# Performance work log

Hardware: AMD Instinct MI355X
Metric: run time of the kernel (lower is better)

The kernel has to match this reference:

```python
import jax, jax.numpy as jnp
import numpy as np

B, T, D, H = 2, 2048, 1024, 16
HD = D // H  # head_dim = 64
ROPE_BASE = 10000.0


def _rope_cos_sin(seq_len, head_dim, dtype):
    # Llama-style RoPE tables: [T, head_dim] with freqs repeated over both halves
    inv_freq = 1.0 / (ROPE_BASE ** (jnp.arange(0, head_dim, 2, dtype=jnp.float32) / head_dim))
    t = jnp.arange(seq_len, dtype=jnp.float32)
    freqs = jnp.outer(t, inv_freq)            # [T, head_dim/2]
    emb = jnp.concatenate([freqs, freqs], -1)  # [T, head_dim]
    return jnp.cos(emb).astype(dtype), jnp.sin(emb).astype(dtype)


def _apply_rope(x, cos, sin):
    # x: [B, T, H, HD]; rotate-half convention
    d2 = x.shape[-1] // 2
    x1, x2 = x[..., :d2], x[..., d2:]
    rotated = jnp.concatenate([-x2, x1], axis=-1)
    c = cos[None, :, None, :]
    s = sin[None, :, None, :]
    return x * c + rotated * s


def setup_inputs() -> dict:
    key = jax.random.key(0)
    ks = jax.random.split(key, 5)
    scale = 0.02
    return {
        "x": jax.random.normal(ks[0], (B, T, D), dtype=jnp.float32),
        "w_q": jax.random.normal(ks[1], (D, D), dtype=jnp.float32) * scale,
        "w_k": jax.random.normal(ks[2], (D, D), dtype=jnp.float32) * scale,
        "w_v": jax.random.normal(ks[3], (D, D), dtype=jnp.float32) * scale,
        "w_o": jax.random.normal(ks[4], (D, D), dtype=jnp.float32) * scale,
    }


def reference(x, w_q, w_k, w_v, w_o):
    b, n, d_in = x.shape
    # QKV projections -> [b, n, H, HD]
    q = (x @ w_q).reshape(b, n, H, HD)
    k = (x @ w_k).reshape(b, n, H, HD)
    v = (x @ w_v).reshape(b, n, H, HD)
    cos, sin = _rope_cos_sin(n, HD, x.dtype)
    q = _apply_rope(q, cos, sin)
    k = _apply_rope(k, cos, sin)
    # causal attention, scores scaled by sqrt(head_dim)
    scores = jnp.einsum('bqhd,bkhd->bhqk', q, k) / jnp.sqrt(jnp.asarray(HD, x.dtype))
    causal = jnp.tril(jnp.ones((n, n), dtype=bool))
    scores = jnp.where(causal[None, None, :, :], scores, -jnp.inf)
    weights = jax.nn.softmax(scores, axis=-1)
    ctx = jnp.einsum('bhqk,bkhd->bqhd', weights, v).reshape(b, n, H * HD)
    return ctx @ w_o
```

## Files before the change

### kernel.cpp

```cpp
#include <hip/hip_runtime.h>
#include <hip/hip_bf16.h>
#include <cstdint>

using u16 = unsigned short;
typedef short bf16x8 __attribute__((ext_vector_type(8)));
typedef float f32x4 __attribute__((ext_vector_type(4)));
typedef float f32x16 __attribute__((ext_vector_type(16)));
typedef u16 u16x4 __attribute__((ext_vector_type(4)));
typedef u16 u16x8 __attribute__((ext_vector_type(8)));

__device__ __forceinline__ u16 f2bf(float f) {
  union { float f; uint32_t u; } v; v.f = f;
  uint32_t r = (v.u + 0x7fffu + ((v.u >> 16) & 1u)) >> 16;
  return (u16)r;
}

__device__ __forceinline__ float bf2f(u16 u) {
  union { uint32_t u; float f; } v; v.u = (uint32_t)u << 16; return v.f;
}

__device__ __forceinline__ void async16(const void* g, void* l) {
  __builtin_amdgcn_global_load_lds(
      (const __attribute__((address_space(1))) uint32_t*)g,
      (__attribute__((address_space(3))) uint32_t*)l, 16, 0, 0);
}

__device__ __forceinline__ uint32_t cvtpk(float a, float b) {
  uint32_t r;
  asm("v_cvt_pk_bf16_f32 %0, %1, %2" : "=v"(r) : "v"(a), "v"(b));
  return r;
}

__device__ __forceinline__ void plswap(uint32_t& a, uint32_t& b) {
  asm volatile("v_permlane32_swap_b32 %0, %1" : "+v"(a), "+v"(b));
}

__global__ __launch_bounds__(256) void prep_kernel(
    const float* __restrict__ x, const float* __restrict__ wq, const float* __restrict__ wk,
    const float* __restrict__ wv, const float* __restrict__ wo,
    u16* __restrict__ xb, u16* __restrict__ Wqt, u16* __restrict__ Wkt,
    u16* __restrict__ Wvt, u16* __restrict__ Wot) {
  __shared__ float tile[64][65];
  const int tid = threadIdx.x;
  const int bid = blockIdx.x;
  if (bid < 4096) {
    int i = (bid * 256 + tid) * 4;
    float4 v = *(const float4*)(x + i);
    u16x4 o;
    o[0] = f2bf(v.x); o[1] = f2bf(v.y); o[2] = f2bf(v.z); o[3] = f2bf(v.w);
    *(u16x4*)(xb + i) = o;
    return;
  }
  const int id = bid - 4096;
  const int wsel = id >> 8, sub = id & 255;
  const float* W = (wsel == 0) ? wq : (wsel == 1) ? wk : (wsel == 2) ? wv : wo;
  u16* Wt = (wsel == 0) ? Wqt : (wsel == 1) ? Wkt : (wsel == 2) ? Wvt : Wot;
  const int k0 = (sub & 15) * 64, n0 = (sub >> 4) * 64;
#pragma unroll
  for (int i = 0; i < 4; ++i) {
    int c = i * 256 + tid;
    int r = c >> 4, c4 = c & 15;
    float4 v = *(const float4*)(W + (size_t)(k0 + r) * 1024 + n0 + c4 * 4);
    tile[r][c4 * 4 + 0] = v.x; tile[r][c4 * 4 + 1] = v.y;
    tile[r][c4 * 4 + 2] = v.z; tile[r][c4 * 4 + 3] = v.w;
  }
  __syncthreads();
#pragma unroll
  for (int i = 0; i < 2; ++i) {
    int c = i * 256 + tid;
    int n = c >> 3, kc = c & 7;
    u16x8 o;
#pragma unroll
    for (int j = 0; j < 8; ++j) o[j] = f2bf(tile[kc * 8 + j][n]);
    *(u16x8*)(Wt + (size_t)(n0 + n) * 1024 + k0 + kc * 8) = o;
  }
}

__device__ __forceinline__ void stage_ab(const u16* A, const u16* Bt, int m0, int n0, int kt,
                                         u16* As, u16* Bs, int w, int lane) {
#pragma unroll
  for (int c = 0; c < 2; ++c) {
    int chunk = w * 128 + c * 64 + lane;
    int row = chunk >> 2, cc = chunk & 3;
    int koff = kt * 32 + ((cc ^ (row & 3)) << 3);
    const u16* ga = A + (size_t)(m0 + row) * 1024 + koff;
    async16(ga, As + (size_t)(w * 128 + c * 64) * 8);
    const u16* gb = Bt + (size_t)(n0 + row) * 1024 + koff;
    async16(gb, Bs + (size_t)(w * 128 + c * 64) * 8);
  }
}

__device__ __forceinline__ void gemm_mainloop(const u16* A, const u16* Bt, int m0, int n0,
                                              u16 (*As)[4096], u16 (*Bs)[4096], f32x4 acc[4][4]) {
  const int tid = threadIdx.x, w = tid >> 6, lane = tid & 63, lo = lane & 15, hi = lane >> 4;
  const int mb = (w >> 1) * 64, nb = (w & 1) * 64;
  stage_ab(A, Bt, m0, n0, 0, As[0], Bs[0], w, lane);
  __syncthreads();
  for (int kt = 0; kt < 32; ++kt) {
    int cur = kt & 1;
    if (kt + 1 < 32) stage_ab(A, Bt, m0, n0, kt + 1, As[cur ^ 1], Bs[cur ^ 1], w, lane);
    bf16x8 af[4], bfr[4];
#pragma unroll
    for (int i = 0; i < 4; ++i) {
      int ra = mb + i * 16 + lo;
      af[i] = *(const bf16x8*)(As[cur] + ra * 32 + ((hi ^ (ra & 3)) << 3));
      int rb = nb + i * 16 + lo;
      bfr[i] = *(const bf16x8*)(Bs[cur] + rb * 32 + ((hi ^ (rb & 3)) << 3));
    }
#pragma unroll
    for (int i = 0; i < 4; ++i)
#pragma unroll
      for (int j = 0; j < 4; ++j)
        acc[i][j] = __builtin_amdgcn_mfma_f32_16x16x32_bf16(af[i], bfr[j], acc[i][j], 0, 0, 0);
    __syncthreads();
  }
}

__global__ __launch_bounds__(256) void qkv_gemm_kernel(
    const u16* __restrict__ xb, const u16* __restrict__ Wcat,
    u16* __restrict__ Qf, u16* __restrict__ Kf, u16* __restrict__ Vf) {
  __shared__ u16 As[2][4096];
  __shared__ u16 Bs[2][4096];
  const int m0 = blockIdx.x * 128, n0 = blockIdx.y * 128;
  const int mode = n0 >> 10, nloc = n0 & 1023;
  f32x4 acc[4][4];
  const f32x4 z4 = {0.f, 0.f, 0.f, 0.f};
#pragma unroll
  for (int i = 0; i < 4; ++i)
#pragma unroll
    for (int j = 0; j < 4; ++j) acc[i][j] = z4;
  gemm_mainloop(xb, Wcat, m0, n0, As, Bs, acc);

  const int tid = threadIdx.x, w = tid >> 6, lane = tid & 63, lo = lane & 15, hi = lane >> 4;
  const int h = (nloc >> 6) + (w & 1);
  const int mrow0 = m0 + (w >> 1) * 64;
  if (mode < 2) {
    u16* Out = (mode == 0) ? Qf : Kf;
    const float qscale = (mode == 0) ? 0.18033688011112042f : 1.0f;
    const float invf0 = exp2f(-(float)lo * 0.41524101186092034f);
    const float invf1 = invf0 * 0.01f;
    const int lnoff = (lo >> 3) * 256 + (lo & 7);
#pragma unroll
    for (int mi = 0; mi < 4; ++mi) {
#pragma unroll
      for (int r = 0; r < 4; ++r) {
        int tg = mrow0 + mi * 16 + hi * 4 + r;
        int b = tg >> 11, tp = tg & 2047;
        float c0, s0, c1, s1;
        __sincosf((float)tp * invf0, &s0, &c0);
        __sincosf((float)tp * invf1, &s1, &c1);
        size_t obase = (size_t)((b * 16 + h) * 64 + (tp >> 5)) * 2048 + (size_t)(tp & 31) * 8 + lnoff;
#pragma unroll
        for (int nf = 0; nf < 4; ++nf) {
          float v = acc[mi][nf][r];
          float rot = (nf < 2) ? -acc[mi][nf + 2][r] : acc[mi][nf - 2][r];
          float cs = (nf & 1) ? c1 : c0;
          float sn = (nf & 1) ? s1 : s0;
          Out[obase + nf * 512] = f2bf((v * cs + rot * sn) * qscale);
        }
      }
    }
  } else {
#pragma unroll
    for (int mi = 0; mi < 4; ++mi) {
      int tg0 = mrow0 + mi * 16 + hi * 4;
      int b = tg0 >> 11, tp0 = tg0 & 2047;
#pragma unroll
      for (int nf = 0; nf < 4; ++nf) {
        int d = nf * 16 + lo;
        u16x4 pk;
#pragma unroll
        for (int r = 0; r < 4; ++r) pk[r] = f2bf(acc[mi][nf][r]);
        *(u16x4*)(Vf + ((size_t)((b * 16 + h) * 256 + (tp0 >> 3)) * 64 + d) * 8 + (tp0 & 7)) = pk;
      }
    }
  }
}

__global__ __launch_bounds__(256, 2) void attn_kernel(const u16* __restrict__ Qf, const u16* __restrict__ Kf,
                                                      const u16* __restrict__ Vf, u16* __restrict__ ctx) {
  __shared__ u16 Omb[3][32 * 68];
  __shared__ float Lsm[3][32];
  const int bh = blockIdx.x, qi = blockIdx.y;
  const int g = (qi & ~7) | (((qi >> 3) & 1) ? (7 - (qi & 7)) : (qi & 7));
  const int tid = threadIdx.x, p = tid >> 6, lane = tid & 63;
  const int lo5 = lane & 31, hi = lane >> 5;
  const int nt = (g >> 1) + 1;
  const int qq = nt >> 2, rem = nt & 3;
  const int cnt = qq + (p < rem ? 1 : 0);
  const int t0 = p * qq + (p < rem ? p : rem);
  const int bb = bh >> 4, h = bh & 15;

  const u16* Qb = Qf + (size_t)bh * 131072 + (size_t)g * 2048 + lane * 8;
  const u16* Kb = Kf + (size_t)bh * 131072 + lane * 8;
  const u16* Vb = Vf + (size_t)bh * 131072 + hi * 512 + lo5 * 8;

  bf16x8 qf[4];
#pragma unroll
  for (int d = 0; d < 4; ++d) qf[d] = *(const bf16x8*)(Qb + d * 512);

  f32x16 O0, O1;
#pragma unroll
  for (int r = 0; r < 16; ++r) { O0[r] = 0.f; O1[r] = 0.f; }
  float l_run = 0.f;

  bf16x8 kA0[4], kB0[4], kA1[4], kB1[4];

  auto LOADK = [&](int t, bf16x8 (&kA)[4], bf16x8 (&kB)[4]) {
    const u16* kt = Kb + (size_t)t * 4096;
#pragma unroll
    for (int d = 0; d < 4; ++d) {
      kA[d] = *(const bf16x8*)(kt + d * 512);
      kB[d] = *(const bf16x8*)(kt + 2048 + d * 512);
    }
  };

  auto COMPUTE = [&](int t, bf16x8 (&kA)[4], bf16x8 (&kB)[4]) {
    f32x16 s0, s1;
#pragma unroll
    for (int r = 0; r < 16; ++r) { s0[r] = 0.f; s1[r] = 0.f; }
    __builtin_amdgcn_s_setprio(1);
#pragma unroll
    for (int d = 0; d < 4; ++d) {
      s0 = __builtin_amdgcn_mfma_f32_32x32x16_bf16(kA[d], qf[d], s0, 0, 0, 0);
      s1 = __builtin_amdgcn_mfma_f32_32x32x16_bf16(kB[d], qf[d], s1, 0, 0, 0);
    }
    __builtin_amdgcn_s_setprio(0);

    const u16* vt = Vb + (size_t)t * 4096;
    bf16x8 vA[4], vB[4];
#pragma unroll
    for (int ks = 0; ks < 4; ++ks) {
      vA[ks] = *(const bf16x8*)(vt + ks * 1024);
      vB[ks] = *(const bf16x8*)(vt + ks * 1024 + 256);
    }

    if (t == nt - 1) {
#pragma unroll
      for (int r = 0; r < 16; ++r) {
        int kl = (r & 3) + 8 * (r >> 2) + 4 * hi;
        if (g & 1) {
          if (kl > lo5) s1[r] = -1e30f;
        } else {
          if (kl > lo5) s0[r] = -1e30f;
          s1[r] = -1e30f;
        }
      }
    }

    float sm[16];
#pragma unroll
    for (int r = 0; r < 16; ++r) {
      float p0 = exp2f(s0[r]); s0[r] = p0;
      float p1 = exp2f(s1[r]); s1[r] = p1;
      sm[r] = p0 + p1;
    }
#pragma unroll
    for (int d = 8; d; d >>= 1)
#pragma unroll
      for (int r = 0; r < d; ++r) sm[r] += sm[r + d];
    l_run += sm[0];

    uint32_t W0[8], W1[8];
#pragma unroll
    for (int i = 0; i < 8; ++i) {
      W0[i] = cvtpk(s0[2 * i], s0[2 * i + 1]);
      W1[i] = cvtpk(s1[2 * i], s1[2 * i + 1]);
    }
    __builtin_amdgcn_s_setprio(1);
#pragma unroll
    for (int ks = 0; ks < 4; ++ks) {
      uint32_t a, d2, c2, e2;
      if (ks == 0)      { a = W0[0]; d2 = W0[1]; c2 = W0[2]; e2 = W0[3]; }
      else if (ks == 1) { a = W0[4]; d2 = W0[5]; c2 = W0[6]; e2 = W0[7]; }
      else if (ks == 2) { a = W1[0]; d2 = W1[1]; c2 = W1[2]; e2 = W1[3]; }
      else              { a = W1[4]; d2 = W1[5]; c2 = W1[6]; e2 = W1[7]; }
      plswap(a, c2);
      plswap(d2, e2);
      union { uint32_t u[4]; bf16x8 v; } f;
      f.u[0] = a; f.u[1] = d2; f.u[2] = c2; f.u[3] = e2;
      O0 = __builtin_amdgcn_mfma_f32_32x32x16_bf16(vA[ks], f.v, O0, 0, 0, 0);
      O1 = __builtin_amdgcn_mfma_f32_32x32x16_bf16(vB[ks], f.v, O1, 0, 0, 0);
    }
    __builtin_amdgcn_s_setprio(0);
  };

  if (cnt > 0) {
    LOADK(t0, kA0, kB0);
    int i = 0;
    for (;;) {
      if (i + 1 < cnt) LOADK(t0 + i + 1, kA1, kB1);
      COMPUTE(t0 + i, kA0, kB0);
      if (++i >= cnt) break;
      if (i + 1 < cnt) LOADK(t0 + i + 1, kA0, kB0);
      COMPUTE(t0 + i, kA1, kB1);
      if (++i >= cnt) break;
    }
  }

  l_run += __shfl_xor(l_run, 32);

  if (p != 0) {
    u16* om = Omb[p - 1] + (size_t)lo5 * 68;
#pragma unroll
    for (int gg = 0; gg < 4; ++gg) {
      int off = 8 * gg + 4 * hi;
      u16x4 w0, w1;
#pragma unroll
      for (int j = 0; j < 4; ++j) { w0[j] = f2bf(O0[4 * gg + j]); w1[j] = f2bf(O1[4 * gg + j]); }
      *(u16x4*)(om + off) = w0;
      *(u16x4*)(om + 32 + off) = w1;
    }
    if (hi == 0) Lsm[p - 1][lo5] = l_run;
  }
  __syncthreads();
  if (p == 0) {
    float invl = 1.0f / (l_run + Lsm[0][lo5] + Lsm[1][lo5] + Lsm[2][lo5]);
    const u16* om1 = Omb[0] + (size_t)lo5 * 68;
    const u16* om2 = Omb[1] + (size_t)lo5 * 68;
    const u16* om3 = Omb[2] + (size_t)lo5 * 68;
    const int tq = 32 * g + lo5;
    size_t rowb = ((size_t)(bb * 2048 + tq)) * 1024 + h * 64;
#pragma unroll
    for (int gg = 0; gg < 4; ++gg) {
      int off = 8 * gg + 4 * hi;
      u16x4 q1 = *(const u16x4*)(om1 + off), q2 = *(const u16x4*)(om2 + off), q3 = *(const u16x4*)(om3 + off);
      u16x4 pk;
#pragma unroll
      for (int j = 0; j < 4; ++j)
        pk[j] = f2bf((O0[4 * gg + j] + bf2f(q1[j]) + bf2f(q2[j]) + bf2f(q3[j])) * invl);
      *(u16x4*)(ctx + rowb + off) = pk;
      u16x4 r1 = *(const u16x4*)(om1 + 32 + off), r2 = *(const u16x4*)(om2 + 32 + off), r3 = *(const u16x4*)(om3 + 32 + off);
#pragma unroll
      for (int j = 0; j < 4; ++j)
        pk[j] = f2bf((O1[4 * gg + j] + bf2f(r1[j]) + bf2f(r2[j]) + bf2f(r3[j])) * invl);
      *(u16x4*)(ctx + rowb + 32 + off) = pk;
    }
  }
}

__global__ __launch_bounds__(256) void out_gemm_kernel(const u16* __restrict__ ctxb,
                                                       const u16* __restrict__ Wot,
                                                       float* __restrict__ out) {
  __shared__ u16 As[2][4096];
  __shared__ u16 Bs[2][4096];
  const int m0 = blockIdx.x * 128, n0 = blockIdx.y * 128;
  f32x4 acc[4][4];
  const f32x4 z4 = {0.f, 0.f, 0.f, 0.f};
#pragma unroll
  for (int i = 0; i < 4; ++i)
#pragma unroll
    for (int j = 0; j < 4; ++j) acc[i][j] = z4;
  gemm_mainloop(ctxb, Wot, m0, n0, As, Bs, acc);
  const int tid = threadIdx.x, w = tid >> 6, lane = tid & 63, lo = lane & 15, hi = lane >> 4;
  const int col0 = n0 + (w & 1) * 64 + lo;
#pragma unroll
  for (int mi = 0; mi < 4; ++mi)
#pragma unroll
    for (int r = 0; r < 4; ++r) {
      int tg = m0 + (w >> 1) * 64 + mi * 16 + hi * 4 + r;
#pragma unroll
      for (int nf = 0; nf < 4; ++nf)
        out[(size_t)tg * 1024 + col0 + nf * 16] = acc[mi][nf][r];
    }
}

extern "C" void kernel_launch(void* const* d_in, const int* in_sizes, int n_in,
                              void* d_out, int out_size, void* d_ws, size_t ws_size,
                              hipStream_t stream) {
  (void)in_sizes; (void)n_in; (void)out_size; (void)ws_size;
  const float* x  = (const float*)d_in[0];
  const float* wq = (const float*)d_in[1];
  const float* wk = (const float*)d_in[2];
  const float* wv = (const float*)d_in[3];
  const float* wo = (const float*)d_in[4];
  char* ws = (char*)d_ws;
  u16* xb   = (u16*)(ws + (size_t)0);
  u16* Wqt  = (u16*)(ws + ((size_t)8  << 20));
  u16* Wkt  = (u16*)(ws + ((size_t)10 << 20));
  u16* Wvt  = (u16*)(ws + ((size_t)12 << 20));
  u16* Wot  = (u16*)(ws + ((size_t)14 << 20));
  u16* Qf   = (u16*)(ws + ((size_t)16 << 20));
  u16* Kf   = (u16*)(ws + ((size_t)24 << 20));
  u16* Vf   = (u16*)(ws + ((size_t)32 << 20));
  u16* ctxb = (u16*)(ws + ((size_t)40 << 20));

  prep_kernel<<<5120, 256, 0, stream>>>(x, wq, wk, wv, wo, xb, Wqt, Wkt, Wvt, Wot);
  qkv_gemm_kernel<<<dim3(32, 24), 256, 0, stream>>>(xb, Wqt, Qf, Kf, Vf);
  attn_kernel<<<dim3(32, 64), 256, 0, stream>>>(Qf, Kf, Vf, ctxb);
  out_gemm_kernel<<<dim3(32, 8), 256, 0, stream>>>(ctxb, Wot, (float*)d_out);
}
```

Before: 115.1 us.

## Use 8 waves per block in QKV and output GEMMs

Both GEMM kernels go from 256 to 512 threads per 128x128 tile. Each wave now computes a 64x32 sub-tile, with its column fragments interleaved so the RoPE pair (d, d+32) stays within one wave. Each thread issues a single async load per operand per k-step. The aim is more waves in flight for latency hiding and fewer accumulator registers per thread. The cost is more LDS fragment reads per MFMA and more barrier participants.

```diff
diff --git a/kernel.cpp b/kernel.cpp
--- a/kernel.cpp
+++ b/kernel.cpp
@@ -76,88 +76,75 @@
   }
 }
 
-__device__ __forceinline__ void stage_ab(const u16* A, const u16* Bt, int m0, int n0, int kt,
-                                         u16* As, u16* Bs, int w, int lane) {
-#pragma unroll
-  for (int c = 0; c < 2; ++c) {
-    int chunk = w * 128 + c * 64 + lane;
-    int row = chunk >> 2, cc = chunk & 3;
-    int koff = kt * 32 + ((cc ^ (row & 3)) << 3);
-    const u16* ga = A + (size_t)(m0 + row) * 1024 + koff;
-    async16(ga, As + (size_t)(w * 128 + c * 64) * 8);
-    const u16* gb = Bt + (size_t)(n0 + row) * 1024 + koff;
-    async16(gb, Bs + (size_t)(w * 128 + c * 64) * 8);
-  }
-}
-
-__device__ __forceinline__ void gemm_mainloop(const u16* A, const u16* Bt, int m0, int n0,
-                                              u16 (*As)[4096], u16 (*Bs)[4096], f32x4 acc[4][4]) {
+__device__ __forceinline__ void stage8(const u16* A, const u16* Bt, int m0, int n0, int kt,
+                                       u16* As, u16* Bs, int tid) {
+  int row = tid >> 2, cc = tid & 3;
+  int koff = kt * 32 + ((cc ^ (row & 3)) << 3);
+  async16(A + (size_t)(m0 + row) * 1024 + koff, As + (size_t)tid * 8);
+  async16(Bt + (size_t)(n0 + row) * 1024 + koff, Bs + (size_t)tid * 8);
+}
+
+__device__ __forceinline__ void gemm_mainloop8(const u16* A, const u16* Bt, int m0, int n0,
+                                               u16 (*As)[4096], u16 (*Bs)[4096], f32x4 acc[4][2]) {
   const int tid = threadIdx.x, w = tid >> 6, lane = tid & 63, lo = lane & 15, hi = lane >> 4;
-  const int mb = (w >> 1) * 64, nb = (w & 1) * 64;
-  stage_ab(A, Bt, m0, n0, 0, As[0], Bs[0], w, lane);
+  const int mb = (w >> 2) * 64;
+  const int cb = ((w >> 1) & 1) * 64 + (w & 1) * 16;
+  stage8(A, Bt, m0, n0, 0, As[0], Bs[0], tid);
   __syncthreads();
   for (int kt = 0; kt < 32; ++kt) {
     int cur = kt & 1;
-    if (kt + 1 < 32) stage_ab(A, Bt, m0, n0, kt + 1, As[cur ^ 1], Bs[cur ^ 1], w, lane);
-    bf16x8 af[4], bfr[4];
-#pragma unroll
-    for (int i = 0; i < 4; ++i) {
-      int ra = mb + i * 16 + lo;
-      af[i] = *(const bf16x8*)(As[cur] + ra * 32 + ((hi ^ (ra & 3)) << 3));
-      int rb = nb + i * 16 + lo;
-      bfr[i] = *(const bf16x8*)(Bs[cur] + rb * 32 + ((hi ^ (rb & 3)) << 3));
-    }
+    if (kt + 1 < 32) stage8(A, Bt, m0, n0, kt + 1, As[cur ^ 1], Bs[cur ^ 1], tid);
+    const int sw = (hi ^ (lo & 3)) << 3;
+    bf16x8 af[4], bfr[2];
+#pragma unroll
+    for (int i = 0; i < 4; ++i) af[i] = *(const bf16x8*)(As[cur] + (mb + i * 16 + lo) * 32 + sw);
+#pragma unroll
+    for (int j = 0; j < 2; ++j) bfr[j] = *(const bf16x8*)(Bs[cur] + (cb + j * 32 + lo) * 32 + sw);
 #pragma unroll
     for (int i = 0; i < 4; ++i)
 #pragma unroll
-      for (int j = 0; j < 4; ++j)
+      for (int j = 0; j < 2; ++j)
         acc[i][j] = __builtin_amdgcn_mfma_f32_16x16x32_bf16(af[i], bfr[j], acc[i][j], 0, 0, 0);
     __syncthreads();
   }
 }
 
-__global__ __launch_bounds__(256) void qkv_gemm_kernel(
+__global__ __launch_bounds__(512, 4) void qkv_gemm_kernel(
     const u16* __restrict__ xb, const u16* __restrict__ Wcat,
     u16* __restrict__ Qf, u16* __restrict__ Kf, u16* __restrict__ Vf) {
   __shared__ u16 As[2][4096];
   __shared__ u16 Bs[2][4096];
   const int m0 = blockIdx.x * 128, n0 = blockIdx.y * 128;
   const int mode = n0 >> 10, nloc = n0 & 1023;
-  f32x4 acc[4][4];
+  f32x4 acc[4][2];
   const f32x4 z4 = {0.f, 0.f, 0.f, 0.f};
 #pragma unroll
   for (int i = 0; i < 4; ++i)
 #pragma unroll
-    for (int j = 0; j < 4; ++j) acc[i][j] = z4;
-  gemm_mainloop(xb, Wcat, m0, n0, As, Bs, acc);
+    for (int j = 0; j < 2; ++j) acc[i][j] = z4;
+  gemm_mainloop8(xb, Wcat, m0, n0, As, Bs, acc);
 
   const int tid = threadIdx.x, w = tid >> 6, lane = tid & 63, lo = lane & 15, hi = lane >> 4;
-  const int h = (nloc >> 6) + (w & 1);
-  const int mrow0 = m0 + (w >> 1) * 64;
+  const int c1 = (w >> 1) & 1, c2 = w & 1;
+  const int h = (nloc >> 6) + c1;
+  const int mrow0 = m0 + (w >> 2) * 64;
   if (mode < 2) {
     u16* Out = (mode == 0) ? Qf : Kf;
     const float qscale = (mode == 0) ? 0.18033688011112042f : 1.0f;
-    const float invf0 = exp2f(-(float)lo * 0.41524101186092034f);
-    const float invf1 = invf0 * 0.01f;
-    const int lnoff = (lo >> 3) * 256 + (lo & 7);
+    const float invf = exp2f(-(float)(c2 * 16 + lo) * 0.41524101186092034f);
+    const int lnoff = (lo >> 3) * 256 + (lo & 7) + c2 * 512;
 #pragma unroll
     for (int mi = 0; mi < 4; ++mi) {
 #pragma unroll
       for (int r = 0; r < 4; ++r) {
         int tg = mrow0 + mi * 16 + hi * 4 + r;
         int b = tg >> 11, tp = tg & 2047;
-        float c0, s0, c1, s1;
-        __sincosf((float)tp * invf0, &s0, &c0);
-        __sincosf((float)tp * invf1, &s1, &c1);
+        float cs, sn;
+        __sincosf((float)tp * invf, &sn, &cs);
         size_t obase = (size_t)((b * 16 + h) * 64 + (tp >> 5)) * 2048 + (size_t)(tp & 31) * 8 + lnoff;
-#pragma unroll
-        for (int nf = 0; nf < 4; ++nf) {
-          float v = acc[mi][nf][r];
-          float rot = (nf < 2) ? -acc[mi][nf + 2][r] : acc[mi][nf - 2][r];
-          float cs = (nf & 1) ? c1 : c0;
-          float sn = (nf & 1) ? s1 : s0;
-          Out[obase + nf * 512] = f2bf((v * cs + rot * sn) * qscale);
-        }
+        float v0 = acc[mi][0][r], v1 = acc[mi][1][r];
+        Out[obase]        = f2bf((v0 * cs - v1 * sn) * qscale);
+        Out[obase + 1024] = f2bf((v1 * cs + v0 * sn) * qscale);
       }
     }
   } else {
@@ -166,11 +153,11 @@
       int tg0 = mrow0 + mi * 16 + hi * 4;
       int b = tg0 >> 11, tp0 = tg0 & 2047;
 #pragma unroll
-      for (int nf = 0; nf < 4; ++nf) {
-        int d = nf * 16 + lo;
+      for (int j = 0; j < 2; ++j) {
+        int d = c2 * 16 + j * 32 + lo;
         u16x4 pk;
 #pragma unroll
-        for (int r = 0; r < 4; ++r) pk[r] = f2bf(acc[mi][nf][r]);
+        for (int r = 0; r < 4; ++r) pk[r] = f2bf(acc[mi][j][r]);
         *(u16x4*)(Vf + ((size_t)((b * 16 + h) * 256 + (tp0 >> 3)) * 64 + d) * 8 + (tp0 & 7)) = pk;
       }
     }
@@ -339,29 +326,28 @@
   }
 }
 
-__global__ __launch_bounds__(256) void out_gemm_kernel(const u16* __restrict__ ctxb,
-                                                       const u16* __restrict__ Wot,
-                                                       float* __restrict__ out) {
+__global__ __launch_bounds__(512, 4) void out_gemm_kernel(const u16* __restrict__ ctxb,
+                                                          const u16* __restrict__ Wot,
+                                                          float* __restrict__ out) {
   __shared__ u16 As[2][4096];
   __shared__ u16 Bs[2][4096];
   const int m0 = blockIdx.x * 128, n0 = blockIdx.y * 128;
-  f32x4 acc[4][4];
+  f32x4 acc[4][2];
   const f32x4 z4 = {0.f, 0.f, 0.f, 0.f};
 #pragma unroll
   for (int i = 0; i < 4; ++i)
 #pragma unroll
-    for (int j = 0; j < 4; ++j) acc[i][j] = z4;
-  gemm_mainloop(ctxb, Wot, m0, n0, As, Bs, acc);
+    for (int j = 0; j < 2; ++j) acc[i][j] = z4;
+  gemm_mainloop8(ctxb, Wot, m0, n0, As, Bs, acc);
   const int tid = threadIdx.x, w = tid >> 6, lane = tid & 63, lo = lane & 15, hi = lane >> 4;
-  const int col0 = n0 + (w & 1) * 64 + lo;
+  const int colb = n0 + ((w >> 1) & 1) * 64 + (w & 1) * 16;
 #pragma unroll
   for (int mi = 0; mi < 4; ++mi)
 #pragma unroll
     for (int r = 0; r < 4; ++r) {
-      int tg = m0 + (w >> 1) * 64 + mi * 16 + hi * 4 + r;
-#pragma unroll
-      for (int nf = 0; nf < 4; ++nf)
-        out[(size_t)tg * 1024 + col0 + nf * 16] = acc[mi][nf][r];
+      int tg = m0 + (w >> 2) * 64 + mi * 16 + hi * 4 + r;
+      out[(size_t)tg * 1024 + colb + lo] = acc[mi][0][r];
+      out[(size_t)tg * 1024 + colb + 32 + lo] = acc[mi][1][r];
     }
 }
 
@@ -386,7 +372,7 @@
   u16* ctxb = (u16*)(ws + ((size_t)40 << 20));
 
   prep_kernel<<<5120, 256, 0, stream>>>(x, wq, wk, wv, wo, xb, Wqt, Wkt, Wvt, Wot);
-  qkv_gemm_kernel<<<dim3(32, 24), 256, 0, stream>>>(xb, Wqt, Qf, Kf, Vf);
+  qkv_gemm_kernel<<<dim3(32, 24), 512, 0, stream>>>(xb, Wqt, Qf, Kf, Vf);
   attn_kernel<<<dim3(32, 64), 256, 0, stream>>>(Qf, Kf, Vf, ctxb);
-  out_gemm_kernel<<<dim3(32, 8), 256, 0, stream>>>(ctxb, Wot, (float*)d_out);
-}
+  out_gemm_kernel<<<dim3(32, 8), 512, 0, stream>>>(ctxb, Wot, (float*)d_out);
+}
```

After: 106.1 us (median of 2 runs). 1.09x faster.
